# Performance work log

Hardware: AMD Instinct MI355X
Metric: run time of the kernel (lower is better)

Reference implementation:

```python
import jax, jax.numpy as jnp
import numpy as np

M, IN, OUT = 8192, 4096, 4096
BLOCK_N, BLOCK_K = 128, 128
NB = IN // BLOCK_K  # 32 in-blocks
INT8_MAX = 127.0
EPS = 1e-6


def setup_inputs() -> dict:
    key = jax.random.key(0)
    k1, k2, k3, k4 = jax.random.split(key, 4)
    x = jax.random.normal(k1, (M, IN), dtype=jnp.float32)
    # pre-quantized int8 weights, layout [output_size, input_size]
    weight_q = jax.random.randint(k2, (OUT, IN), -128, 128, dtype=jnp.int8)
    # block-wise scales, kernel-ready layout [in_blocks, 1, output_size]
    weight_scale = (jax.random.uniform(k3, (NB, 1, OUT), dtype=jnp.float32) + 0.5) * 0.01
    bias = jax.random.normal(k4, (OUT,), dtype=jnp.float32)
    return {"x": x, "weight_q": weight_q, "weight_scale": weight_scale, "bias": bias}


def _quantize_activation(x):
    # dynamic per-token symmetric int8 quantization
    amax = jnp.max(jnp.abs(x), axis=-1, keepdims=True)          # [M, 1]
    x_scale = jnp.maximum(amax, EPS) / INT8_MAX                  # [M, 1]
    x_q = jnp.clip(jnp.round(x / x_scale), -128.0, 127.0)        # [M, IN]
    return x_q, x_scale


def reference(x, weight_q, weight_scale, bias):
    # x: [M, IN]; weight_q: [OUT, IN] int8; weight_scale: [NB, 1, OUT]; bias: [OUT]
    x_q, x_scale = _quantize_activation(x)
    # Dequantize weights block-wise along K: scale for column k, row n is
    # weight_scale[k // BLOCK_K, 0, n].
    ws = weight_scale[:, 0, :].T                                 # [OUT, NB]
    w_deq = (weight_q.astype(jnp.float32).reshape(OUT, NB, BLOCK_K)
             * ws[:, :, None]).reshape(OUT, IN)                  # [OUT, IN] fp32
    # quantized matmul + dequant by activation scale
    out = jnp.einsum('mk,nk->mn', x_q, w_deq) * x_scale          # [M, OUT]
    out = out + bias
    return out
```

## Files before the change

kernel.cpp:

```cpp
#include <hip/hip_runtime.h>
#include <cstdint>

#define M_DIM 8192
#define K_DIM 4096
#define N_DIM 4096
#define NBLK 32
#define BLK  128

typedef int   v4i __attribute__((ext_vector_type(4)));
typedef float v4f __attribute__((ext_vector_type(4)));

__device__ __forceinline__ void gload_lds16(const void* g, void* l) {
  __builtin_amdgcn_global_load_lds(
      (const __attribute__((address_space(1))) void*)g,
      (__attribute__((address_space(3))) void*)l, 16, 0, 0);
}

__global__ __launch_bounds__(256) void pack_w(
    const int* __restrict__ w32, int* __restrict__ w8) {
  const size_t i = (size_t)blockIdx.x * 256 + threadIdx.x;
  const int4 v = ((const int4*)w32)[i];
  w8[i] = (v.x & 255) | ((v.y & 255) << 8) | ((v.z & 255) << 16) | ((v.w & 255) << 24);
}

__global__ __launch_bounds__(256) void quant_rows(
    const float* __restrict__ x, int8_t* __restrict__ xq, float* __restrict__ xs) {
  const int row = blockIdx.x;
  const int tid = threadIdx.x;
  const float4* xr = (const float4*)(x + (size_t)row * K_DIM);

  float4 v[4];
  float amax = 0.f;
#pragma unroll
  for (int i = 0; i < 4; ++i) {
    v[i] = xr[i * 256 + tid];
    amax = fmaxf(amax, fmaxf(fmaxf(fabsf(v[i].x), fabsf(v[i].y)),
                             fmaxf(fabsf(v[i].z), fabsf(v[i].w))));
  }
#pragma unroll
  for (int off = 32; off > 0; off >>= 1)
    amax = fmaxf(amax, __shfl_xor(amax, off, 64));

  __shared__ float red[4];
  if ((tid & 63) == 0) red[tid >> 6] = amax;
  __syncthreads();
  amax = fmaxf(fmaxf(red[0], red[1]), fmaxf(red[2], red[3]));
  amax = fmaxf(amax, 1e-6f);
  const float s = amax / 127.0f;
  if (tid == 0) xs[row] = s;

  int* xqo = (int*)(xq + (size_t)row * K_DIM);
#pragma unroll
  for (int i = 0; i < 4; ++i) {
    int q0 = (int)fminf(fmaxf(rintf(v[i].x / s), -128.f), 127.f);
    int q1 = (int)fminf(fmaxf(rintf(v[i].y / s), -128.f), 127.f);
    int q2 = (int)fminf(fmaxf(rintf(v[i].z / s), -128.f), 127.f);
    int q3 = (int)fminf(fmaxf(rintf(v[i].w / s), -128.f), 127.f);
    xqo[i * 256 + tid] =
        (q0 & 255) | ((q1 & 255) << 8) | ((q2 & 255) << 16) | ((q3 & 255) << 24);
  }
}

__global__ __launch_bounds__(256) void gemm_q8(
    const int8_t* __restrict__ xq, const int8_t* __restrict__ wq,
    const float* __restrict__ wscale, const float* __restrict__ xs,
    const float* __restrict__ bias, float* __restrict__ out) {
  __shared__ int8_t lA[128 * 128];
  __shared__ int8_t lB[128 * 128];

  const int tid = threadIdx.x;
  const int m0 = blockIdx.x * 128;
  const int n0 = blockIdx.y * 128;

  const int srow   = tid >> 3;
  const int schunk = (tid & 7) ^ (srow & 7);
  const int8_t* ga = xq + (size_t)(m0 + srow) * K_DIM + schunk * 16;
  const int8_t* gb = wq + (size_t)(n0 + srow) * K_DIM + schunk * 16;
  int8_t* la_dst = lA + tid * 16;
  int8_t* lb_dst = lB + tid * 16;

  const int lane = tid & 63;
  const int wv = tid >> 6;
  const int wm = (wv & 1) << 6;
  const int wn = (wv >> 1) << 6;
  const int lr = lane & 15;
  const int lq = lane >> 4;

  int a_off[4][2], b_off[4][2];
#pragma unroll
  for (int i = 0; i < 4; ++i) {
#pragma unroll
    for (int h = 0; h < 2; ++h) {
      const int ch = (h << 2) | lq;
      const int rowA = wm + i * 16 + lr;
      const int rowB = wn + i * 16 + lr;
      a_off[i][h] = rowA * 128 + ((ch ^ (rowA & 7)) << 4);
      b_off[i][h] = rowB * 128 + ((ch ^ (rowB & 7)) << 4);
    }
  }

  v4f facc[4][4];
#pragma unroll
  for (int i = 0; i < 4; ++i)
#pragma unroll
    for (int j = 0; j < 4; ++j) facc[i][j] = {0.f, 0.f, 0.f, 0.f};

  const float* wsp = wscale + n0 + wn;

  for (int kb = 0; kb < NBLK; ++kb) {
    __syncthreads();
#pragma unroll
    for (int p = 0; p < 4; ++p) {
      gload_lds16(ga + (size_t)p * 32 * K_DIM, la_dst + p * 4096);
      gload_lds16(gb + (size_t)p * 32 * K_DIM, lb_dst + p * 4096);
    }
    ga += BLK;
    gb += BLK;
    __syncthreads();

    v4i iacc[4][4];
#pragma unroll
    for (int i = 0; i < 4; ++i)
#pragma unroll
      for (int j = 0; j < 4; ++j) iacc[i][j] = {0, 0, 0, 0};

#pragma unroll
    for (int h = 0; h < 2; ++h) {
      v4i af[4], bf[4];
#pragma unroll
      for (int i = 0; i < 4; ++i) af[i] = *(const v4i*)(lA + a_off[i][h]);
#pragma unroll
      for (int j = 0; j < 4; ++j) bf[j] = *(const v4i*)(lB + b_off[j][h]);
#pragma unroll
      for (int i = 0; i < 4; ++i)
#pragma unroll
        for (int j = 0; j < 4; ++j)
          iacc[i][j] = __builtin_amdgcn_mfma_i32_16x16x64_i8(af[i], bf[j],
                                                             iacc[i][j], 0, 0, 0);
    }

    const float* wsk = wsp + kb * N_DIM;
#pragma unroll
    for (int j = 0; j < 4; ++j) {
      const float wsv = wsk[j * 16 + lr];
#pragma unroll
      for (int i = 0; i < 4; ++i)
#pragma unroll
        for (int r = 0; r < 4; ++r)
          facc[i][j][r] += wsv * (float)iacc[i][j][r];
    }
  }

  float bv[4];
#pragma unroll
  for (int j = 0; j < 4; ++j) bv[j] = bias[n0 + wn + j * 16 + lr];
#pragma unroll
  for (int i = 0; i < 4; ++i) {
    const int mb = m0 + wm + i * 16 + (lq << 2);
#pragma unroll
    for (int r = 0; r < 4; ++r) {
      const float sc = xs[mb + r];
      float* op = out + (size_t)(mb + r) * N_DIM + n0 + wn + lr;
#pragma unroll
      for (int j = 0; j < 4; ++j) op[j * 16] = facc[i][j][r] * sc + bv[j];
    }
  }
}

extern "C" void kernel_launch(void* const* d_in, const int* in_sizes, int n_in,
                              void* d_out, int out_size, void* d_ws, size_t ws_size,
                              hipStream_t stream) {
  const float* x      = (const float*)d_in[0];
  const int*   w32    = (const int*)d_in[1];
  const float* wscale = (const float*)d_in[2];
  const float* bias   = (const float*)d_in[3];
  float* out = (float*)d_out;

  int8_t* xq  = (int8_t*)d_ws;
  int8_t* wq8 = (int8_t*)d_ws + (size_t)M_DIM * K_DIM;
  float*  xs  = (float*)((char*)d_ws + (size_t)M_DIM * K_DIM + (size_t)N_DIM * K_DIM);

  pack_w<<<(N_DIM * (size_t)K_DIM / 4 + 255) / 256, 256, 0, stream>>>(w32, (int*)wq8);
  quant_rows<<<M_DIM, 256, 0, stream>>>(x, xq, xs);
  dim3 grid(M_DIM / 128, N_DIM / 128);
  gemm_q8<<<grid, 256, 0, stream>>>(xq, wq8, wscale, xs, bias, out);
}
```

Measured before the change: 487.4 us.

## Split GEMM tile across eight waves and quantize with a reciprocal multiply

The int8 GEMM block grows from 256 to 512 threads. Each of the 8 waves now computes a 32x64 sub-tile instead of a 64x64 one, and the integer accumulators are kept per output column group rather than as a full 4x4 array. This lowers register pressure and gives each compute unit more waves to hide LDS and global latency. The per-block weight scales are now loaded before the barrier, and the activation quantization multiplies by a precomputed reciprocal instead of dividing, which can change rounding on a few borderline values.

```diff
diff --git a/kernel.cpp b/kernel.cpp
--- a/kernel.cpp
+++ b/kernel.cpp
@@ -46,22 +46,23 @@
   __syncthreads();
   amax = fmaxf(fmaxf(red[0], red[1]), fmaxf(red[2], red[3]));
   amax = fmaxf(amax, 1e-6f);
-  const float s = amax / 127.0f;
+  const float s   = amax / 127.0f;
+  const float inv = 127.0f / amax;
   if (tid == 0) xs[row] = s;
 
   int* xqo = (int*)(xq + (size_t)row * K_DIM);
 #pragma unroll
   for (int i = 0; i < 4; ++i) {
-    int q0 = (int)fminf(fmaxf(rintf(v[i].x / s), -128.f), 127.f);
-    int q1 = (int)fminf(fmaxf(rintf(v[i].y / s), -128.f), 127.f);
-    int q2 = (int)fminf(fmaxf(rintf(v[i].z / s), -128.f), 127.f);
-    int q3 = (int)fminf(fmaxf(rintf(v[i].w / s), -128.f), 127.f);
+    int q0 = (int)fminf(fmaxf(rintf(v[i].x * inv), -128.f), 127.f);
+    int q1 = (int)fminf(fmaxf(rintf(v[i].y * inv), -128.f), 127.f);
+    int q2 = (int)fminf(fmaxf(rintf(v[i].z * inv), -128.f), 127.f);
+    int q3 = (int)fminf(fmaxf(rintf(v[i].w * inv), -128.f), 127.f);
     xqo[i * 256 + tid] =
         (q0 & 255) | ((q1 & 255) << 8) | ((q2 & 255) << 16) | ((q3 & 255) << 24);
   }
 }
 
-__global__ __launch_bounds__(256) void gemm_q8(
+__global__ __launch_bounds__(512) void gemm_q8(
     const int8_t* __restrict__ xq, const int8_t* __restrict__ wq,
     const float* __restrict__ wscale, const float* __restrict__ xs,
     const float* __restrict__ bias, float* __restrict__ out) {
@@ -81,73 +82,70 @@
 
   const int lane = tid & 63;
   const int wv = tid >> 6;
-  const int wm = (wv & 1) << 6;
-  const int wn = (wv >> 1) << 6;
+  const int wm = (wv & 3) << 5;
+  const int wn = (wv >> 2) << 6;
   const int lr = lane & 15;
   const int lq = lane >> 4;
 
-  int a_off[4][2], b_off[4][2];
+  int a_off[2][2], b_off[4][2];
 #pragma unroll
-  for (int i = 0; i < 4; ++i) {
+  for (int h = 0; h < 2; ++h) {
+    const int ch = (h << 2) | lq;
 #pragma unroll
-    for (int h = 0; h < 2; ++h) {
-      const int ch = (h << 2) | lq;
+    for (int i = 0; i < 2; ++i) {
       const int rowA = wm + i * 16 + lr;
-      const int rowB = wn + i * 16 + lr;
       a_off[i][h] = rowA * 128 + ((ch ^ (rowA & 7)) << 4);
-      b_off[i][h] = rowB * 128 + ((ch ^ (rowB & 7)) << 4);
+    }
+#pragma unroll
+    for (int j = 0; j < 4; ++j) {
+      const int rowB = wn + j * 16 + lr;
+      b_off[j][h] = rowB * 128 + ((ch ^ (rowB & 7)) << 4);
     }
   }
 
-  v4f facc[4][4];
+  v4f facc[2][4];
 #pragma unroll
-  for (int i = 0; i < 4; ++i)
+  for (int i = 0; i < 2; ++i)
 #pragma unroll
     for (int j = 0; j < 4; ++j) facc[i][j] = {0.f, 0.f, 0.f, 0.f};
 
-  const float* wsp = wscale + n0 + wn;
+  const float* wsp = wscale + n0 + wn + lr;
 
   for (int kb = 0; kb < NBLK; ++kb) {
+    float wsv[4];
+#pragma unroll
+    for (int j = 0; j < 4; ++j) wsv[j] = wsp[(size_t)kb * N_DIM + j * 16];
+
     __syncthreads();
 #pragma unroll
-    for (int p = 0; p < 4; ++p) {
-      gload_lds16(ga + (size_t)p * 32 * K_DIM, la_dst + p * 4096);
-      gload_lds16(gb + (size_t)p * 32 * K_DIM, lb_dst + p * 4096);
+    for (int p = 0; p < 2; ++p) {
+      gload_lds16(ga + (size_t)p * 64 * K_DIM, la_dst + p * 8192);
+      gload_lds16(gb + (size_t)p * 64 * K_DIM, lb_dst + p * 8192);
     }
     ga += BLK;
     gb += BLK;
     __syncthreads();
 
-    v4i iacc[4][4];
+    v4i af[2][2];
 #pragma unroll
-    for (int i = 0; i < 4; ++i)
+    for (int i = 0; i < 2; ++i)
 #pragma unroll
-      for (int j = 0; j < 4; ++j) iacc[i][j] = {0, 0, 0, 0};
+      for (int h = 0; h < 2; ++h) af[i][h] = *(const v4i*)(lA + a_off[i][h]);
 
 #pragma unroll
-    for (int h = 0; h < 2; ++h) {
-      v4i af[4], bf[4];
+    for (int j = 0; j < 4; ++j) {
+      const v4i b0 = *(const v4i*)(lB + b_off[j][0]);
+      const v4i b1 = *(const v4i*)(lB + b_off[j][1]);
+      v4i i0 = {0, 0, 0, 0}, i1 = {0, 0, 0, 0};
+      i0 = __builtin_amdgcn_mfma_i32_16x16x64_i8(af[0][0], b0, i0, 0, 0, 0);
+      i1 = __builtin_amdgcn_mfma_i32_16x16x64_i8(af[1][0], b0, i1, 0, 0, 0);
+      i0 = __builtin_amdgcn_mfma_i32_16x16x64_i8(af[0][1], b1, i0, 0, 0, 0);
+      i1 = __builtin_amdgcn_mfma_i32_16x16x64_i8(af[1][1], b1, i1, 0, 0, 0);
 #pragma unroll
-      for (int i = 0; i < 4; ++i) af[i] = *(const v4i*)(lA + a_off[i][h]);
-#pragma unroll
-      for (int j = 0; j < 4; ++j) bf[j] = *(const v4i*)(lB + b_off[j][h]);
-#pragma unroll
-      for (int i = 0; i < 4; ++i)
-#pragma unroll
-        for (int j = 0; j < 4; ++j)
-          iacc[i][j] = __builtin_amdgcn_mfma_i32_16x16x64_i8(af[i], bf[j],
-                                                             iacc[i][j], 0, 0, 0);
-    }
-
-    const float* wsk = wsp + kb * N_DIM;
-#pragma unroll
-    for (int j = 0; j < 4; ++j) {
-      const float wsv = wsk[j * 16 + lr];
-#pragma unroll
-      for (int i = 0; i < 4; ++i)
-#pragma unroll
-        for (int r = 0; r < 4; ++r)
-          facc[i][j][r] += wsv * (float)iacc[i][j][r];
+      for (int r = 0; r < 4; ++r) {
+        facc[0][j][r] += wsv[j] * (float)i0[r];
+        facc[1][j][r] += wsv[j] * (float)i1[r];
+      }
     }
   }
 
@@ -155,7 +153,7 @@
 #pragma unroll
   for (int j = 0; j < 4; ++j) bv[j] = bias[n0 + wn + j * 16 + lr];
 #pragma unroll
-  for (int i = 0; i < 4; ++i) {
+  for (int i = 0; i < 2; ++i) {
     const int mb = m0 + wm + i * 16 + (lq << 2);
 #pragma unroll
     for (int r = 0; r < 4; ++r) {
@@ -183,5 +181,5 @@
   pack_w<<<(N_DIM * (size_t)K_DIM / 4 + 255) / 256, 256, 0, stream>>>(w32, (int*)wq8);
   quant_rows<<<M_DIM, 256, 0, stream>>>(x, xq, xs);
   dim3 grid(M_DIM / 128, N_DIM / 128);
-  gemm_q8<<<grid, 256, 0, stream>>>(xq, wq8, wscale, xs, bias, out);
+  gemm_q8<<<grid, 512, 0, stream>>>(xq, wq8, wscale, xs, bias, out);
 }
```

Measured after the change: 465.2 us. -4.5%, faster.
